# Kernel optimization log

Measured on AMD Instinct MI355X. Metric: run time of the kernel, lower is better.

Reference implementation:

```python
import jax, jax.numpy as jnp
import numpy as np

S = 1024; VOCAB = 100000; EMB = 300
POS_SZ = 64; CHAR_E = 50; CHAR_ENC = 128; WLEN = 16
NCHARS = 100; NPOSTAG = 50; NPOSITIONS = 1024
D = EMB + 3 * POS_SZ + CHAR_ENC  # word_rep_size = 620
BIH = 128   # per-direction LSTM hidden (bilstm_hidden_size // 2)
TLH = 256; LCC = 128; GCC = 256
NET = 8; NTAGS = 16; NREL = 16
TOKF = 2 * BIH + LCC + TLH       # 640
SENTF = 2 * TOKF + GCC           # 1536

def _p(k, shape):
    return 0.02 * jax.random.normal(k, shape, dtype=jnp.float32)

def setup_inputs():
    key = jax.random.key(0)
    ks = jax.random.split(key, 30)
    return {
        'word_inputs': jax.random.randint(ks[0], (1, S), 0, VOCAB),
        'char_inputs': jax.random.randint(ks[1], (1, S, WLEN), 0, NCHARS),
        'postag_inputs': jax.random.randint(ks[2], (1, S), 0, NPOSTAG),
        'dependency_inputs': jax.random.randint(ks[3], (1, S), 0, 64),
        'position_inputs': jax.random.randint(ks[4], (1, S), 0, NPOSITIONS),
        'topo_order': jnp.arange(S),  # children-before-parents order
        'parent': jnp.concatenate([jnp.arange(1, S), jnp.array([S])]),  # chain dep tree; root -> dummy slot S
        'pointed_token_idx': 5,
        'word_table': _p(ks[5], (VOCAB, EMB)),
        'char_table': _p(ks[6], (NCHARS, CHAR_E)),
        'char_conv_w': _p(ks[7], (CHAR_ENC, CHAR_E, 3)),
        'char_conv_b': jnp.zeros((CHAR_ENC,), jnp.float32),
        'postag_table': _p(ks[8], (NPOSTAG, POS_SZ)),
        'position_table': _p(ks[9], (NPOSITIONS, POS_SZ)),
        'lstm_f_Wx': _p(ks[10], (D, 4 * BIH)),
        'lstm_f_Wh': _p(ks[11], (BIH, 4 * BIH)),
        'lstm_f_b': jnp.zeros((4 * BIH,), jnp.float32),
        'lstm_b_Wx': _p(ks[12], (D, 4 * BIH)),
        'lstm_b_Wh': _p(ks[13], (BIH, 4 * BIH)),
        'lstm_b_b': jnp.zeros((4 * BIH,), jnp.float32),
        'word_cnn_w': _p(ks[14], (LCC, D, 3)),
        'word_cnn_b': jnp.zeros((LCC,), jnp.float32),
        'tl_Wiou': _p(ks[15], (D, 3 * TLH)),
        'tl_Uiou': _p(ks[16], (TLH, 3 * TLH)),
        'tl_biou': jnp.zeros((3 * TLH,), jnp.float32),
        'tl_Wf': _p(ks[17], (D, TLH)),
        'tl_Uf': _p(ks[18], (TLH, TLH)),
        'tl_bf': jnp.zeros((TLH,), jnp.float32),
        'sent_cnn_w': _p(ks[19], (GCC, D, 3)),
        'sent_cnn_b': jnp.zeros((GCC,), jnp.float32),
        'et_w': _p(ks[20], (GCC + TOKF, NET)),
        'et_b': jnp.zeros((NET,), jnp.float32),
        'crf_w': _p(ks[21], (SENTF, NTAGS)),
        'crf_b': jnp.zeros((NTAGS,), jnp.float32),
        'crf_trans': _p(ks[22], (NTAGS, NTAGS)),
        'rel_w': _p(ks[23], (SENTF, NREL)),
        'rel_b': jnp.zeros((NREL,), jnp.float32),
    }

def _conv1d(x, w, b):
    # x: [N, Cin, W], w: [Cout, Cin, K], padding=1 (matches nn.Conv1d(..., padding=1))
    y = jax.lax.conv_general_dilated(x, w, (1,), [(1, 1)], dimension_numbers=('NCW', 'OIW', 'NCW'))
    return y + b[None, :, None]

def _lstm(xs, Wx, Wh, b):
    H = Wh.shape[0]
    def step(carry, x):
        h, c = carry
        g = x @ Wx + h @ Wh + b
        i, f, gg, o = jnp.split(g, 4, axis=-1)
        c = jax.nn.sigmoid(f) * c + jax.nn.sigmoid(i) * jnp.tanh(gg)
        h = jax.nn.sigmoid(o) * jnp.tanh(c)
        return (h, c), h
    init = (jnp.zeros((H,), xs.dtype), jnp.zeros((H,), xs.dtype))
    _, hs = jax.lax.scan(step, init, xs)
    return hs

def _tree_lstm(x, order, parent, Wiou, Uiou, biou, Wf, Uf, bf):
    # ChildSum TreeLSTM over the whole dependency tree in topological order.
    # Equivalent to the source's per-token subtree recursion: each node's h
    # only depends on its subtree.
    Sn, H = x.shape[0], Uf.shape[0]
    xiou = x @ Wiou + biou                 # [S, 3H]
    xf = jnp.concatenate([x @ Wf + bf, jnp.zeros((1, H), x.dtype)], axis=0)  # dummy row for root's parent
    def step(carry, j):
        h, hsum, fcsum = carry
        iou = xiou[j] + hsum[j] @ Uiou
        i, o, u = jnp.split(iou, 3)
        cj = jax.nn.sigmoid(i) * jnp.tanh(u) + fcsum[j]
        hj = jax.nn.sigmoid(o) * jnp.tanh(cj)
        p = parent[j]
        f = jax.nn.sigmoid(xf[p] + hj @ Uf)  # per-child forget gate
        return (h.at[j].set(hj), hsum.at[p].add(hj), fcsum.at[p].add(f * cj)), None
    h0 = jnp.zeros((Sn, H), x.dtype)
    acc0 = jnp.zeros((Sn + 1, H), x.dtype)
    (h, _, _), _ = jax.lax.scan(step, (h0, acc0, acc0), order)
    return h

def _viterbi(emissions, trans):
    # emissions: [S, T]; trans[i, j] = score(i -> j)
    def step(score, e):
        s = score[:, None] + trans
        return jnp.max(s, axis=0) + e, jnp.argmax(s, axis=0)
    final, ptrs = jax.lax.scan(step, emissions[0], emissions[1:])
    last = jnp.argmax(final)
    def bt(tag, p):
        prev = p[tag]
        return prev, prev
    _, prevs = jax.lax.scan(bt, last, ptrs, reverse=True)
    return jnp.concatenate([prevs, last[None]])

def reference(word_inputs, char_inputs, postag_inputs, dependency_inputs, position_inputs, topo_order, parent, pointed_token_idx, word_table, char_table, char_conv_w, char_conv_b, postag_table, position_table, lstm_f_Wx, lstm_f_Wh, lstm_f_b, lstm_b_Wx, lstm_b_Wh, lstm_b_b, word_cnn_w, word_cnn_b, tl_Wiou, tl_Uiou, tl_biou, tl_Wf, tl_Uf, tl_bf, sent_cnn_w, sent_cnn_b, et_w, et_b, crf_w, crf_b, crf_trans, rel_w, rel_b):
    we = word_table[word_inputs]                                   # [1,S,EMB]
    cx = jnp.transpose(char_table[char_inputs[0]], (0, 2, 1))      # [S,CHAR_E,WLEN]
    ce = jnp.max(jax.nn.relu(_conv1d(cx, char_conv_w, char_conv_b)), axis=-1)[None]  # CharCNN -> [1,S,CHAR_ENC]
    pe = postag_table[postag_inputs]
    poe = position_table[position_inputs]
    de = position_table[dependency_inputs]                         # faithful to source bug: uses position table
    inputs = jnp.concatenate([we, ce, pe, poe, de], axis=-1)       # [1,S,D]
    x = inputs[0]
    hf = _lstm(x, lstm_f_Wx, lstm_f_Wh, lstm_f_b)
    hb = _lstm(x[::-1], lstm_b_Wx, lstm_b_Wh, lstm_b_b)[::-1]
    bilstm = jnp.concatenate([hf, hb], axis=-1)[None]              # [1,S,2*BIH]
    xc = jnp.transpose(inputs, (0, 2, 1))                          # [1,D,S]
    local_cnn = jnp.transpose(_conv1d(xc, word_cnn_w, word_cnn_b), (0, 2, 1))
    tree_h = _tree_lstm(x, topo_order, parent, tl_Wiou, tl_Uiou, tl_biou, tl_Wf, tl_Uf, tl_bf)[None]
    global_cnn = jnp.transpose(jnp.max(_conv1d(xc, sent_cnn_w, sent_cnn_b), axis=-1, keepdims=True), (0, 2, 1))  # [1,1,GCC]
    tokens_info = jnp.concatenate([bilstm, local_cnn, tree_h], axis=-1)  # [1,S,TOKF]
    ptr = tokens_info[:, pointed_token_idx, :]                     # [1,TOKF]
    ptr_info = jnp.broadcast_to(ptr[:, None, :], (1, S, TOKF))
    glob_info = jnp.broadcast_to(global_cnn, (1, S, GCC))
    sentence_encoding = jnp.concatenate([tokens_info, ptr_info, glob_info], axis=-1)  # dropout = identity (eval)
    one_vec = jnp.concatenate([global_cnn[:, 0, :], ptr], axis=-1)
    entitytype = jax.nn.softmax(one_vec @ et_w + et_b, axis=-1)
    entities = _viterbi(sentence_encoding[0] @ crf_w + crf_b, crf_trans)
    relations = jax.nn.sigmoid(sentence_encoding @ rel_w + rel_b)
    return sentence_encoding, entitytype, entities, relations
```

## Files before the change

kernel.cpp:

```cpp
#include <hip/hip_runtime.h>
#include <math.h>

#define SEQ   1024
#define DX    620
#define BIH   128
#define TLH   256
#define NTAGS 16

#define O_X      0
#define O_XGF    634880
#define O_XGB    (O_XGF + 524288)
#define O_XIOU   (O_XGB + 524288)
#define O_XF     (O_XIOU + 786432)
#define O_LCNN   (O_XF + 262400)
#define O_SCNN   (O_LCNN + 131072)
#define O_PART   (O_SCNN + 262144)
#define O_GCNN   (O_PART + 4096)
#define O_HF     (O_GCNN + 256)
#define O_HB     (O_HF + 131072)
#define O_TREEH  (O_HB + 131072)
#define O_IOUA   (O_TREEH + 262144)
#define O_FCSUM  (O_IOUA + 787200)
#define O_EMIS   (O_FCSUM + 262400)
#define O_CNT    (O_EMIS + 16384)

#define SENT 0xFFFFFFFFu

__device__ __forceinline__ float sig_f(float x){ return 1.0f/(1.0f + __expf(-x)); }
__device__ __forceinline__ float tanh_f(float x){
  float ax = fabsf(x);
  float e  = __expf(-2.0f*ax);
  float t  = (1.0f - e)/(1.0f + e);
  return x < 0.0f ? -t : t;
}
__device__ __forceinline__ int physslot(int s){ return s ^ ((s>>3)&7); }

__global__ __launch_bounds__(128) void k_embed(
    const int* __restrict__ wi, const int* __restrict__ ci,
    const int* __restrict__ postag_in, const int* __restrict__ dep_in, const int* __restrict__ pos_in,
    const float* __restrict__ word_table, const float* __restrict__ char_table,
    const float* __restrict__ ccw, const float* __restrict__ ccb,
    const float* __restrict__ postag_table, const float* __restrict__ position_table,
    float* __restrict__ x)
{
  int s = blockIdx.x;
  int tid = threadIdx.x;
  __shared__ __align__(16) float ce[50][16];
  for (int idx = tid; idx < 800; idx += 128){
    int e = idx >> 4, t = idx & 15;
    ce[e][t] = char_table[ci[s*16 + t]*50 + e];
  }
  __syncthreads();
  float* xr = x + (size_t)s*DX;
  const float* wrow = word_table + (size_t)wi[s]*300;
  for (int d = tid; d < 300; d += 128) xr[d] = wrow[d];
  {
    int oc = tid;
    const float* wp = ccw + oc*150;
    float acc[16];
    float b = ccb[oc];
    #pragma unroll
    for (int t=0;t<16;t++) acc[t] = b;
    for (int ic=0; ic<50; ic++){
      float w0 = wp[ic*3+0], w1 = wp[ic*3+1], w2 = wp[ic*3+2];
      float cv[16];
      float4 c0 = *(const float4*)&ce[ic][0];
      float4 c1 = *(const float4*)&ce[ic][4];
      float4 c2 = *(const float4*)&ce[ic][8];
      float4 c3 = *(const float4*)&ce[ic][12];
      cv[0]=c0.x;cv[1]=c0.y;cv[2]=c0.z;cv[3]=c0.w;
      cv[4]=c1.x;cv[5]=c1.y;cv[6]=c1.z;cv[7]=c1.w;
      cv[8]=c2.x;cv[9]=c2.y;cv[10]=c2.z;cv[11]=c2.w;
      cv[12]=c3.x;cv[13]=c3.y;cv[14]=c3.z;cv[15]=c3.w;
      #pragma unroll
      for (int t=0;t<16;t++){
        float a = cv[t]*w1;
        if (t > 0)  a += cv[t-1]*w0;
        if (t < 15) a += cv[t+1]*w2;
        acc[t] += a;
      }
    }
    float m = acc[0];
    #pragma unroll
    for (int t=1;t<16;t++) m = fmaxf(m, acc[t]);
    xr[300 + oc] = fmaxf(m, 0.0f);
  }
  if (tid < 64){
    int d = tid;
    xr[428 + d] = postag_table[postag_in[s]*64 + d];
    xr[492 + d] = position_table[pos_in[s]*64 + d];
    xr[556 + d] = position_table[dep_in[s]*64 + d];
  }
}

__device__ __forceinline__ void gemm_tile(
    const float* __restrict__ x, const float* __restrict__ Bm,
    const float* __restrict__ bias, float* __restrict__ C,
    int N, int K, int amode, int bx, int by, int tid,
    float (*As)[64], float (*Bs)[64], int agentc)
{
  int bn = bx*64, bm = by*64;
  int lane = tid & 63, kg = tid >> 6;
  int tx = tid & 15, ty = tid >> 4;
  float acc[4][4] = {{0.f}};
  for (int k0 = 0; k0 < K; k0 += 20){
    #pragma unroll
    for (int kk=0; kk<5; kk++){
      int k = kg*5 + kk;
      float av;
      if (amode == 0){
        av = x[(size_t)(bm+lane)*DX + k0 + k];
      } else {
        int kc = k0 + k;
        int d  = kc/3;
        int sh = kc - d*3 - 1;
        int row = bm + lane + sh;
        av = (row >= 0 && row < SEQ) ? x[(size_t)row*DX + d] : 0.0f;
      }
      As[k][lane] = av;
      Bs[k][lane] = (amode==0) ? Bm[(size_t)(k0+k)*N + bn + lane]
                               : Bm[(size_t)(bn+lane)*K + k0 + k];
    }
    __syncthreads();
    #pragma unroll
    for (int k=0;k<20;k++){
      float4 a = *(const float4*)&As[k][ty<<2];
      float4 b = *(const float4*)&Bs[k][tx<<2];
      acc[0][0]+=a.x*b.x; acc[0][1]+=a.x*b.y; acc[0][2]+=a.x*b.z; acc[0][3]+=a.x*b.w;
      acc[1][0]+=a.y*b.x; acc[1][1]+=a.y*b.y; acc[1][2]+=a.y*b.z; acc[1][3]+=a.y*b.w;
      acc[2][0]+=a.z*b.x; acc[2][1]+=a.z*b.y; acc[2][2]+=a.z*b.z; acc[2][3]+=a.z*b.w;
      acc[3][0]+=a.w*b.x; acc[3][1]+=a.w*b.y; acc[3][2]+=a.w*b.z; acc[3][3]+=a.w*b.w;
    }
    __syncthreads();
  }
  float4 bb;
  bb.x = bias[bn+(tx<<2)+0]; bb.y = bias[bn+(tx<<2)+1];
  bb.z = bias[bn+(tx<<2)+2]; bb.w = bias[bn+(tx<<2)+3];
  #pragma unroll
  for (int i=0;i<4;i++){
    int row = bm + (ty<<2) + i;
    float v0 = acc[i][0]+bb.x, v1 = acc[i][1]+bb.y, v2 = acc[i][2]+bb.z, v3 = acc[i][3]+bb.w;
    if (agentc){
      float* p = &C[(size_t)row*N + bn + (tx<<2)];
      __hip_atomic_store(p+0, v0, __ATOMIC_RELAXED, __HIP_MEMORY_SCOPE_AGENT);
      __hip_atomic_store(p+1, v1, __ATOMIC_RELAXED, __HIP_MEMORY_SCOPE_AGENT);
      __hip_atomic_store(p+2, v2, __ATOMIC_RELAXED, __HIP_MEMORY_SCOPE_AGENT);
      __hip_atomic_store(p+3, v3, __ATOMIC_RELAXED, __HIP_MEMORY_SCOPE_AGENT);
    } else {
      float4 o; o.x=v0; o.y=v1; o.z=v2; o.w=v3;
      *(float4*)&C[(size_t)row*N + bn + (tx<<2)] = o;
    }
  }
}

__global__ __launch_bounds__(256) void k_gmax1(const float* __restrict__ scnn, float* __restrict__ part){
  int b = blockIdx.x, c = threadIdx.x;
  float m = -3.0e38f;
  for (int s = b*64; s < b*64 + 64; s++) m = fmaxf(m, scnn[(size_t)s*256 + c]);
  part[b*256 + c] = m;
}
__global__ __launch_bounds__(256) void k_gmax2(const float* __restrict__ part, float* __restrict__ gcnn){
  int c = threadIdx.x;
  float m = -3.0e38f;
  for (int b=0; b<16; b++) m = fmaxf(m, part[b*256 + c]);
  gcnn[c] = m;
}

struct RGemm {
  const float* B[4];
  const float* bias[4];
  float*       C[4];
  int          N[4];
};

__global__ __launch_bounds__(256, 1) void k_recur(
    const float* __restrict__ xg_f, const float* __restrict__ xg_b,
    const float* __restrict__ Wh_f, const float* __restrict__ Wh_b,
    const float* __restrict__ xiou, const float* __restrict__ xf,
    const float* __restrict__ Uiou, const float* __restrict__ Uf,
    const int* __restrict__ order, const int* __restrict__ parent,
    float* __restrict__ hf, float* __restrict__ hb,
    float* tree_h, float* iou_acc, float* fcsum,
    const float* __restrict__ x, RGemm rg_args,
    const float* __restrict__ wcnn_w, const float* __restrict__ wcnn_b,
    const float* __restrict__ scnn_w, const float* __restrict__ scnn_b,
    float* __restrict__ lcnn, float* __restrict__ scnn,
    int* cnt)
{
  int bid = blockIdx.x;
  int tid = threadIdx.x;

  if (bid >= 262){
    __shared__ __align__(16) float As[20][64];
    __shared__ __align__(16) float Bs[20][64];
    int j = bid - 262;
    for (int s=0;s<3;s++){
      int tn = j*3 + s;
      if (tn < 32) gemm_tile(x, wcnn_w, wcnn_b, lcnn, 128, 1860, 1, tn&1, tn>>1, tid, As, Bs, 0);
      else { int t2 = tn-32; gemm_tile(x, scnn_w, scnn_b, scnn, 256, 1860, 1, t2&3, t2>>2, tid, As, Bs, 0); }
      __syncthreads();
    }
    return;
  }

  if (bid >= 6){
    __shared__ __align__(16) float As[20][64];
    __shared__ __align__(16) float Bs[20][64];
    int j = bid - 6;
    for (int s=0;s<2;s++){
      int T = j*2 + s;
      int k = T>>5, r = T&31;
      int z, by, bn;
      if (r < 8)       { z=0; by=k;    bn=r;    }
      else if (r < 16) { z=1; by=15-k; bn=r-8;  }
      else if (r < 28) { z=2; by=k;    bn=r-16; }
      else             { z=3; by=k;    bn=r-28; }
      gemm_tile(x, rg_args.B[z], rg_args.bias[z], rg_args.C[z], rg_args.N[z],
                620, 0, bn, by, tid, As, Bs, 1);
      __syncthreads();
      if (tid == 0)
        __hip_atomic_fetch_add(&cnt[z*16 + by], 1, __ATOMIC_RELEASE, __HIP_MEMORY_SCOPE_AGENT);
      __syncthreads();
    }
    return;
  }

  if (bid >= 4){
    const float* xg  = (bid == 4) ? xg_f : xg_b;
    const float* Wh  = (bid == 4) ? Wh_f : Wh_b;
    float* hout      = (bid == 4) ? hf : hb;
    int zc = (bid == 4) ? 0 : 1;
    int cg = tid >> 1, rg = tid & 1;
    float4 w[4][16];
    #pragma unroll
    for (int cc=0;cc<4;cc++){
      int col = cg*4 + cc;
      #pragma unroll
      for (int r4=0;r4<16;r4++){
        int row = rg*64 + r4*4;
        w[cc][r4].x = Wh[(size_t)(row+0)*512 + col];
        w[cc][r4].y = Wh[(size_t)(row+1)*512 + col];
        w[cc][r4].z = Wh[(size_t)(row+2)*512 + col];
        w[cc][r4].w = Wh[(size_t)(row+3)*512 + col];
      }
    }
    #pragma unroll
    for (int cc=0;cc<4;cc++)
      #pragma unroll
      for (int r4=0;r4<16;r4++)
        asm volatile("" : "+v"(w[cc][r4].x), "+v"(w[cc][r4].y), "+v"(w[cc][r4].z), "+v"(w[cc][r4].w));

    __shared__ __align__(16) float lhl[BIH];
    __shared__ float lcst[BIH];
    __shared__ float gl[512];
    if (tid < BIH){ lhl[tid] = 0.f; lcst[tid] = 0.f; }
    __syncthreads();
    const float4* lhl4 = (const float4*)lhl;

    int Wm = (bid == 4) ? -1 : 16;
    {
      int n0 = (bid == 4) ? 0 : (SEQ-1);
      int g0 = n0 >> 6;
      if (bid == 4){
        for (int g = Wm+1; g <= g0; g++)
          while (__hip_atomic_load(&cnt[zc*16+g], __ATOMIC_ACQUIRE, __HIP_MEMORY_SCOPE_AGENT) < 8)
            __builtin_amdgcn_s_sleep(8);
      } else {
        for (int g = Wm-1; g >= g0; g--)
          while (__hip_atomic_load(&cnt[zc*16+g], __ATOMIC_ACQUIRE, __HIP_MEMORY_SCOPE_AGENT) < 8)
            __builtin_amdgcn_s_sleep(8);
      }
      Wm = g0;
    }
    float4 nxg4 = make_float4(0.f,0.f,0.f,0.f);
    if (rg == 0){
      int n0 = (bid == 4) ? 0 : (SEQ-1);
      nxg4 = *(const float4*)&xg[(size_t)n0*512 + cg*4];
    }
    for (int st=0; st<SEQ; st++){
      int n = (bid == 4) ? st : (SEQ-1-st);
      float4 xg4 = nxg4;
      if (st+1 < SEQ){
        int n1 = (bid == 4) ? (st+1) : (SEQ-2-st);
        int g1 = n1 >> 6;
        if (bid == 4){
          if (g1 > Wm){
            for (int g = Wm+1; g <= g1; g++)
              while (__hip_atomic_load(&cnt[zc*16+g], __ATOMIC_ACQUIRE, __HIP_MEMORY_SCOPE_AGENT) < 8)
                __builtin_amdgcn_s_sleep(8);
            Wm = g1;
          }
        } else {
          if (g1 < Wm){
            for (int g = Wm-1; g >= g1; g--)
              while (__hip_atomic_load(&cnt[zc*16+g], __ATOMIC_ACQUIRE, __HIP_MEMORY_SCOPE_AGENT) < 8)
                __builtin_amdgcn_s_sleep(8);
            Wm = g1;
          }
        }
        if (rg == 0) nxg4 = *(const float4*)&xg[(size_t)n1*512 + cg*4];
      }
      float acc[4] = {0.f,0.f,0.f,0.f};
      #pragma unroll
      for (int r4=0;r4<16;r4++){
        float4 h4 = lhl4[rg*16 + r4];
        #pragma unroll
        for (int cc=0;cc<4;cc++)
          acc[cc] += h4.x*w[cc][r4].x + h4.y*w[cc][r4].y + h4.z*w[cc][r4].z + h4.w*w[cc][r4].w;
      }
      #pragma unroll
      for (int cc=0;cc<4;cc++) acc[cc] += __shfl_xor(acc[cc], 1);
      if (rg == 0){
        float4 o = make_float4(acc[0]+xg4.x, acc[1]+xg4.y, acc[2]+xg4.z, acc[3]+xg4.w);
        *(float4*)&gl[cg*4] = o;
      }
      __syncthreads();
      if (tid < BIH){
        float gi = gl[tid], gf = gl[BIH+tid], gg = gl[2*BIH+tid], go = gl[3*BIH+tid];
        float c = sig_f(gf)*lcst[tid] + sig_f(gi)*tanh_f(gg);
        float h = sig_f(go)*tanh_f(c);
        lcst[tid] = c;
        lhl[tid] = h;
        hout[(size_t)n*BIH + tid] = h;
      }
      __syncthreads();
    }
    return;
  }

  int blk = bid;
  int cg = tid >> 3, rg = tid & 7;
  int ulo = blk*64;
  float4 w[8][8];
  #pragma unroll
  for (int cc=0;cc<8;cc++){
    int c = cg*8 + cc;
    const float* Wsrc; size_t stride; int gcol;
    if (c < 192){ Wsrc = Uiou; stride = 768; gcol = (c>>6)*TLH + ulo + (c&63); }
    else        { Wsrc = Uf;   stride = 256; gcol = ulo + (c-192); }
    #pragma unroll
    for (int r4=0;r4<8;r4++){
      int row = rg*32 + r4*4;
      w[cc][r4].x = Wsrc[(size_t)(row+0)*stride + gcol];
      w[cc][r4].y = Wsrc[(size_t)(row+1)*stride + gcol];
      w[cc][r4].z = Wsrc[(size_t)(row+2)*stride + gcol];
      w[cc][r4].w = Wsrc[(size_t)(row+3)*stride + gcol];
    }
  }
  #pragma unroll
  for (int cc=0;cc<8;cc++)
    #pragma unroll
    for (int r4=0;r4<8;r4++)
      asm volatile("" : "+v"(w[cc][r4].x), "+v"(w[cc][r4].y), "+v"(w[cc][r4].z), "+v"(w[cc][r4].w));

  __shared__ __align__(16) float hl[TLH];
  __shared__ float colsum[TLH];
  __shared__ float cprev[64];
  __shared__ int ord_l[SEQ];
  __shared__ int par_l[SEQ];
  for (int i=tid; i<SEQ; i+=256){ ord_l[i] = order[i]; par_l[i] = parent[i]; }
  __syncthreads();
  const float4* hl4 = (const float4*)hl;

  int Wm = -1;
  float nxi=0.f, nxo=0.f, nxu=0.f, nxf=0.f;
  if (tid < 64){
    int n0 = ord_l[0];
    int need = n0 >> 6;
    for (int g = 0; g <= need; g++){
      while (__hip_atomic_load(&cnt[32+g], __ATOMIC_ACQUIRE, __HIP_MEMORY_SCOPE_AGENT) < 12)
        __builtin_amdgcn_s_sleep(8);
      while (__hip_atomic_load(&cnt[48+g], __ATOMIC_ACQUIRE, __HIP_MEMORY_SCOPE_AGENT) < 4)
        __builtin_amdgcn_s_sleep(8);
    }
    Wm = need;
    int uu = ulo + tid;
    nxi = xiou[(size_t)n0*768 + uu];
    nxo = xiou[(size_t)n0*768 + 256 + uu];
    nxu = xiou[(size_t)n0*768 + 512 + uu];
  }

  for (int t=0; t<SEQ; t++){
    int n  = ord_l[t];
    int m  = (t > 0) ? ord_l[t-1] : 0;
    int pp = (t > 0) ? par_l[m] : -1;
    bool ppeq = (pp == n);

    float xi=nxi, xo=nxo, xu=nxu, xfv=nxf;
    float ac_i=0.f, ac_o=0.f, ac_u=0.f, fcn=0.f;
    float po_i=0.f, po_o=0.f, po_u=0.f, po_f=0.f;
    if (tid < 64){
      int uu = ulo + tid;
      if (t+1 < SEQ){
        int n1 = ord_l[t+1];
        int pr = par_l[n];
        int need = n1 >> 6;
        if (pr < SEQ && (pr>>6) > need) need = pr>>6;
        if (need > Wm){
          for (int g = Wm+1; g <= need; g++){
            while (__hip_atomic_load(&cnt[32+g], __ATOMIC_ACQUIRE, __HIP_MEMORY_SCOPE_AGENT) < 12)
              __builtin_amdgcn_s_sleep(8);
            while (__hip_atomic_load(&cnt[48+g], __ATOMIC_ACQUIRE, __HIP_MEMORY_SCOPE_AGENT) < 4)
              __builtin_amdgcn_s_sleep(8);
          }
          Wm = need;
        }
        nxi = xiou[(size_t)n1*768 + uu];
        nxo = xiou[(size_t)n1*768 + 256 + uu];
        nxu = xiou[(size_t)n1*768 + 512 + uu];
        nxf = xf[(size_t)pr*256 + uu];
      }
      ac_i = iou_acc[(size_t)n*768 + uu];
      ac_o = iou_acc[(size_t)n*768 + 256 + uu];
      ac_u = iou_acc[(size_t)n*768 + 512 + uu];
      fcn  = fcsum[(size_t)n*256 + uu];
      if (t > 0 && !ppeq){
        po_i = iou_acc[(size_t)pp*768 + uu];
        po_o = iou_acc[(size_t)pp*768 + 256 + uu];
        po_u = iou_acc[(size_t)pp*768 + 512 + uu];
        po_f = fcsum[(size_t)pp*256 + uu];
      }
    }

    if (t > 0){
      float acc[8] = {0.f,0.f,0.f,0.f,0.f,0.f,0.f,0.f};
      int base = rg << 3;
      #pragma unroll
      for (int r4=0;r4<8;r4++){
        float4 h4 = hl4[base + (r4 ^ rg)];
        #pragma unroll
        for (int cc=0;cc<8;cc++)
          acc[cc] += h4.x*w[cc][r4].x + h4.y*w[cc][r4].y + h4.z*w[cc][r4].z + h4.w*w[cc][r4].w;
      }
      #pragma unroll
      for (int cc=0;cc<8;cc++){
        acc[cc] += __shfl_xor(acc[cc], 1);
        acc[cc] += __shfl_xor(acc[cc], 2);
        acc[cc] += __shfl_xor(acc[cc], 4);
      }
      if (rg == 0){
        *(float4*)&colsum[cg*8]     = make_float4(acc[0], acc[1], acc[2], acc[3]);
        *(float4*)&colsum[cg*8 + 4] = make_float4(acc[4], acc[5], acc[6], acc[7]);
      }
    }
    __syncthreads();

    if (tid < 64){
      int uu = ulo + tid;
      float ai = ac_i, ao = ac_o, au = ac_u, fcs = fcn;
      if (t > 0){
        float vi = colsum[tid], vo = colsum[64+tid], vuu = colsum[128+tid], vf = colsum[192+tid];
        float fg  = sig_f(xfv + vf);
        float fcc = fg * cprev[tid];
        if (ppeq){
          ai += vi; ao += vo; au += vuu; fcs += fcc;
        } else {
          iou_acc[(size_t)pp*768 + uu]       = po_i + vi;
          iou_acc[(size_t)pp*768 + 256 + uu] = po_o + vo;
          iou_acc[(size_t)pp*768 + 512 + uu] = po_u + vuu;
          fcsum[(size_t)pp*256 + uu]         = po_f + fcc;
        }
      }
      float cc = sig_f(xi + ai)*tanh_f(xu + au) + fcs;
      float hh = sig_f(xo + ao)*tanh_f(cc);
      cprev[tid] = cc;
      int s = uu >> 2;
      hl[physslot(s)*4 + (uu & 3)] = hh;
      __hip_atomic_store(&tree_h[(size_t)n*TLH + uu], hh, __ATOMIC_RELAXED, __HIP_MEMORY_SCOPE_AGENT);
    } else {
      int p  = tid - 64;
      int fi = (p < ulo) ? p : p + 64;
      const unsigned* tp = (const unsigned*)(tree_h + (size_t)n*TLH + fi);
      unsigned v = __hip_atomic_load(tp, __ATOMIC_RELAXED, __HIP_MEMORY_SCOPE_AGENT);
      while (v == SENT){
        __builtin_amdgcn_s_sleep(1);
        v = __hip_atomic_load(tp, __ATOMIC_RELAXED, __HIP_MEMORY_SCOPE_AGENT);
      }
      hl[physslot(fi>>2)*4 + (fi&3)] = __uint_as_float(v);
    }
    __syncthreads();
  }
}

__global__ __launch_bounds__(256) void k_assemble(
    const float* __restrict__ hf, const float* __restrict__ hb,
    const float* __restrict__ lcnn, const float* __restrict__ tree_h,
    const float* __restrict__ gcnn,
    const float* __restrict__ crf_w, const float* __restrict__ crf_b,
    const float* __restrict__ rel_w, const float* __restrict__ rel_b,
    const int* __restrict__ ptk,
    float* __restrict__ se_out, float* __restrict__ emis, float* __restrict__ rel_out)
{
  int s = blockIdx.x, tid = threadIdx.x;
  int p = ptk[0];
  __shared__ float se[1536];
  for (int d = tid; d < 1536; d += 256){
    float v;
    if      (d < 128)  v = hf[(size_t)s*128 + d];
    else if (d < 256)  v = hb[(size_t)s*128 + d-128];
    else if (d < 384)  v = lcnn[(size_t)s*128 + d-256];
    else if (d < 640)  v = tree_h[(size_t)s*256 + d-384];
    else if (d < 768)  v = hf[(size_t)p*128 + d-640];
    else if (d < 896)  v = hb[(size_t)p*128 + d-768];
    else if (d < 1024) v = lcnn[(size_t)p*128 + d-896];
    else if (d < 1280) v = tree_h[(size_t)p*256 + d-1024];
    else               v = gcnn[d-1280];
    se[d] = v;
    se_out[(size_t)s*1536 + d] = v;
  }
  __syncthreads();
  int o = tid >> 3, l = tid & 7;
  const float* W = (o < 16) ? crf_w : rel_w;
  int oc = (o < 16) ? o : (o - 16);
  float a = 0.f;
  for (int k = l; k < 1536; k += 8) a += se[k]*W[(size_t)k*16 + oc];
  for (int off = 4; off; off >>= 1) a += __shfl_down(a, off, 8);
  if (l == 0){
    if (o < 16) emis[(size_t)s*16 + o] = a + crf_b[o];
    else        rel_out[(size_t)s*16 + oc] = sig_f(a + rel_b[oc]);
  }
}

__global__ __launch_bounds__(256) void k_entity(
    const float* __restrict__ hf, const float* __restrict__ hb,
    const float* __restrict__ lcnn, const float* __restrict__ tree_h,
    const float* __restrict__ gcnn,
    const float* __restrict__ et_w, const float* __restrict__ et_b,
    const int* __restrict__ ptk, float* __restrict__ out_et)
{
  __shared__ float ov[896];
  __shared__ float lg[8];
  int tid = threadIdx.x;
  int p = ptk[0];
  for (int d = tid; d < 896; d += 256){
    float v;
    if      (d < 256) v = gcnn[d];
    else if (d < 384) v = hf[(size_t)p*128 + d-256];
    else if (d < 512) v = hb[(size_t)p*128 + d-384];
    else if (d < 640) v = lcnn[(size_t)p*128 + d-512];
    else              v = tree_h[(size_t)p*256 + d-640];
    ov[d] = v;
  }
  __syncthreads();
  int o = tid >> 5, l = tid & 31;
  float a = 0.f;
  for (int k = l; k < 896; k += 32) a += ov[k]*et_w[(size_t)k*8 + o];
  for (int off = 16; off; off >>= 1) a += __shfl_down(a, off, 32);
  if (l == 0) lg[o] = a + et_b[o];
  __syncthreads();
  if (tid == 0){
    float mx = lg[0];
    for (int i=1;i<8;i++) mx = fmaxf(mx, lg[i]);
    float e[8], sum = 0.f;
    for (int i=0;i<8;i++){ e[i] = __expf(lg[i]-mx); sum += e[i]; }
    for (int i=0;i<8;i++) out_et[i] = e[i]/sum;
  }
}

__global__ __launch_bounds__(64) void k_viterbi(
    const float* __restrict__ emis, const float* __restrict__ trans, float* __restrict__ out_e)
{
  __shared__ __align__(16) float ring[64][16];
  __shared__ unsigned char ptrs[1023*16];
  __shared__ float scL[16];
  int l = threadIdx.x;
  int j = l >> 2, iq = l & 3;
  float tr0 = trans[(iq*4+0)*16 + j];
  float tr1 = trans[(iq*4+1)*16 + j];
  float tr2 = trans[(iq*4+2)*16 + j];
  float tr3 = trans[(iq*4+3)*16 + j];
  {
    const float* src = &emis[(size_t)l*16];
    float4 a = *(const float4*)(src+0), b = *(const float4*)(src+4);
    float4 c = *(const float4*)(src+8), d = *(const float4*)(src+12);
    *(float4*)&ring[l][0] = a;  *(float4*)&ring[l][4] = b;
    *(float4*)&ring[l][8] = c;  *(float4*)&ring[l][12] = d;
  }
  float cur = ring[0][j];
  float sc0 = __shfl(cur, (iq*4+0)<<2, 64);
  float sc1 = __shfl(cur, (iq*4+1)<<2, 64);
  float sc2 = __shfl(cur, (iq*4+2)<<2, 64);
  float sc3 = __shfl(cur, (iq*4+3)<<2, 64);
  float myfinal = cur;
  for (int t=1; t<1024; t++){
    if ((t & 63) == 0){
      const float* src = &emis[(size_t)(t+l)*16];
      float4 a = *(const float4*)(src+0), b = *(const float4*)(src+4);
      float4 c = *(const float4*)(src+8), d = *(const float4*)(src+12);
      int rr = (t+l) & 63;
      *(float4*)&ring[rr][0] = a;  *(float4*)&ring[rr][4] = b;
      *(float4*)&ring[rr][8] = c;  *(float4*)&ring[rr][12] = d;
    }
    float v0 = sc0 + tr0, v1 = sc1 + tr1, v2 = sc2 + tr2, v3 = sc3 + tr3;
    float best = v0; int barg = iq*4;
    if (v1 > best){ best = v1; barg = iq*4+1; }
    if (v2 > best){ best = v2; barg = iq*4+2; }
    if (v3 > best){ best = v3; barg = iq*4+3; }
    float ob = __shfl_down(best, 1, 4); int oa = __shfl_down(barg, 1, 4);
    if (ob > best){ best = ob; barg = oa; }
    ob = __shfl_down(best, 2, 4); oa = __shfl_down(barg, 2, 4);
    if (ob > best){ best = ob; barg = oa; }
    float ns = 0.f;
    if (iq == 0){
      ns = best + ring[t & 63][j];
      ptrs[(t-1)*16 + j] = (unsigned char)barg;
      myfinal = ns;
    }
    sc0 = __shfl(ns, (iq*4+0)<<2, 64);
    sc1 = __shfl(ns, (iq*4+1)<<2, 64);
    sc2 = __shfl(ns, (iq*4+2)<<2, 64);
    sc3 = __shfl(ns, (iq*4+3)<<2, 64);
  }
  if (iq == 0) scL[j] = myfinal;
  if (l == 0){
    float b = scL[0]; int last = 0;
    #pragma unroll
    for (int i=1;i<16;i++){ if (scL[i] > b){ b = scL[i]; last = i; } }
    out_e[1023] = (float)last;
    int cur2 = last;
    for (int t=1022; t>=0; t--){ cur2 = (int)ptrs[t*16 + cur2]; out_e[t] = (float)cur2; }
  }
}

extern "C" void kernel_launch(void* const* d_in, const int* in_sizes, int n_in,
                              void* d_out, int out_size, void* d_ws, size_t ws_size,
                              hipStream_t stream)
{
  (void)in_sizes; (void)n_in; (void)out_size; (void)ws_size;
  const int*   wi         = (const int*)d_in[0];
  const int*   ci         = (const int*)d_in[1];
  const int*   postag_in  = (const int*)d_in[2];
  const int*   dep_in     = (const int*)d_in[3];
  const int*   pos_in     = (const int*)d_in[4];
  const int*   order      = (const int*)d_in[5];
  const int*   parent     = (const int*)d_in[6];
  const int*   ptk        = (const int*)d_in[7];
  const float* word_table = (const float*)d_in[8];
  const float* char_table = (const float*)d_in[9];
  const float* ccw        = (const float*)d_in[10];
  const float* ccb        = (const float*)d_in[11];
  const float* postag_tab = (const float*)d_in[12];
  const float* pos_tab    = (const float*)d_in[13];
  const float* Wx_f       = (const float*)d_in[14];
  const float* Wh_f       = (const float*)d_in[15];
  const float* b_f        = (const float*)d_in[16];
  const float* Wx_b       = (const float*)d_in[17];
  const float* Wh_b       = (const float*)d_in[18];
  const float* b_b        = (const float*)d_in[19];
  const float* wcnn_w     = (const float*)d_in[20];
  const float* wcnn_b     = (const float*)d_in[21];
  const float* Wiou       = (const float*)d_in[22];
  const float* Uiou       = (const float*)d_in[23];
  const float* biou       = (const float*)d_in[24];
  const float* Wf_t       = (const float*)d_in[25];
  const float* Uf_t       = (const float*)d_in[26];
  const float* bf_t       = (const float*)d_in[27];
  const float* scnn_w     = (const float*)d_in[28];
  const float* scnn_b     = (const float*)d_in[29];
  const float* et_w       = (const float*)d_in[30];
  const float* et_b       = (const float*)d_in[31];
  const float* crf_w      = (const float*)d_in[32];
  const float* crf_b      = (const float*)d_in[33];
  const float* crf_trans  = (const float*)d_in[34];
  const float* rel_w      = (const float*)d_in[35];
  const float* rel_b      = (const float*)d_in[36];

  float* ws = (float*)d_ws;
  float* x      = ws + O_X;
  float* xg_f   = ws + O_XGF;
  float* xg_b   = ws + O_XGB;
  float* xiou   = ws + O_XIOU;
  float* xf     = ws + O_XF;
  float* lcnn   = ws + O_LCNN;
  float* scnn   = ws + O_SCNN;
  float* part   = ws + O_PART;
  float* gcnn   = ws + O_GCNN;
  float* hf     = ws + O_HF;
  float* hb     = ws + O_HB;
  float* tree_h = ws + O_TREEH;
  float* iou_acc= ws + O_IOUA;
  float* fcsum  = ws + O_FCSUM;
  float* emis   = ws + O_EMIS;
  int*   cnt    = (int*)(ws + O_CNT);

  float* outF     = (float*)d_out;
  float* se_out   = outF;
  float* et_out   = outF + 1572864;
  float* ent_out  = outF + 1572872;
  float* rel_out  = outF + 1573896;

  hipMemsetAsync(xf, 0, (size_t)1025*256*sizeof(float), stream);
  hipMemsetAsync(iou_acc, 0, ((size_t)1025*768 + 1025*256)*sizeof(float), stream);
  hipMemsetAsync(tree_h, 0xFF, (size_t)1024*256*sizeof(float), stream);
  hipMemsetAsync(cnt, 0, 256, stream);

  k_embed<<<SEQ, 128, 0, stream>>>(wi, ci, postag_in, dep_in, pos_in,
                                   word_table, char_table, ccw, ccb,
                                   postag_tab, pos_tab, x);

  RGemm rga;
  rga.B[0]=Wx_f;  rga.bias[0]=b_f;   rga.C[0]=xg_f; rga.N[0]=512;
  rga.B[1]=Wx_b;  rga.bias[1]=b_b;   rga.C[1]=xg_b; rga.N[1]=512;
  rga.B[2]=Wiou;  rga.bias[2]=biou;  rga.C[2]=xiou; rga.N[2]=768;
  rga.B[3]=Wf_t;  rga.bias[3]=bf_t;  rga.C[3]=xf;   rga.N[3]=256;

  k_recur<<<294, 256, 0, stream>>>(xg_f, xg_b, Wh_f, Wh_b, xiou, xf, Uiou, Uf_t,
                                   order, parent, hf, hb, tree_h, iou_acc, fcsum,
                                   x, rga, wcnn_w, wcnn_b, scnn_w, scnn_b, lcnn, scnn,
                                   cnt);

  k_gmax1<<<16, 256, 0, stream>>>(scnn, part);
  k_gmax2<<<1, 256, 0, stream>>>(part, gcnn);

  k_assemble<<<SEQ, 256, 0, stream>>>(hf, hb, lcnn, tree_h, gcnn,
                                      crf_w, crf_b, rel_w, rel_b, ptk,
                                      se_out, emis, rel_out);

  k_entity<<<1, 256, 0, stream>>>(hf, hb, lcnn, tree_h, gcnn, et_w, et_b, ptk, et_out);

  k_viterbi<<<1, 64, 0, stream>>>(emis, crf_trans, ent_out);
}
```

Measured before the change: 2.717 ms.

## Fuse embedding and global max into persistent recurrent kernel with counter-based dataflow

Moves the embedding computation into the persistent k_recur kernel as extra blocks that publish per-64-token completion counters. The input-projection and CNN GEMM tiles now wait on those counters instead of a kernel boundary, so the recurrences can start as soon as their first token groups are ready. The global max-pool becomes a single block inside the same kernel that waits on a CNN tile counter. The entity softmax is folded into k_assemble as an extra block. Together these remove several launches and let work overlap across stages, at the cost of more spin-waits and a grid of 807 blocks that relies on forward progress of the producer blocks.

```diff
diff --git a/kernel.cpp b/kernel.cpp
--- a/kernel.cpp
+++ b/kernel.cpp
@@ -24,6 +24,13 @@
 #define O_EMIS   (O_FCSUM + 262400)
 #define O_CNT    (O_EMIS + 16384)
 
+#define C_XGF  0
+#define C_XGB  16
+#define C_XIOU 32
+#define C_XF   48
+#define C_X    64
+#define C_SCNN 80
+
 #define SENT 0xFFFFFFFFu
 
 __device__ __forceinline__ float sig_f(float x){ return 1.0f/(1.0f + __expf(-x)); }
@@ -35,62 +42,9 @@
 }
 __device__ __forceinline__ int physslot(int s){ return s ^ ((s>>3)&7); }
 
-__global__ __launch_bounds__(128) void k_embed(
-    const int* __restrict__ wi, const int* __restrict__ ci,
-    const int* __restrict__ postag_in, const int* __restrict__ dep_in, const int* __restrict__ pos_in,
-    const float* __restrict__ word_table, const float* __restrict__ char_table,
-    const float* __restrict__ ccw, const float* __restrict__ ccb,
-    const float* __restrict__ postag_table, const float* __restrict__ position_table,
-    float* __restrict__ x)
-{
-  int s = blockIdx.x;
-  int tid = threadIdx.x;
-  __shared__ __align__(16) float ce[50][16];
-  for (int idx = tid; idx < 800; idx += 128){
-    int e = idx >> 4, t = idx & 15;
-    ce[e][t] = char_table[ci[s*16 + t]*50 + e];
-  }
-  __syncthreads();
-  float* xr = x + (size_t)s*DX;
-  const float* wrow = word_table + (size_t)wi[s]*300;
-  for (int d = tid; d < 300; d += 128) xr[d] = wrow[d];
-  {
-    int oc = tid;
-    const float* wp = ccw + oc*150;
-    float acc[16];
-    float b = ccb[oc];
-    #pragma unroll
-    for (int t=0;t<16;t++) acc[t] = b;
-    for (int ic=0; ic<50; ic++){
-      float w0 = wp[ic*3+0], w1 = wp[ic*3+1], w2 = wp[ic*3+2];
-      float cv[16];
-      float4 c0 = *(const float4*)&ce[ic][0];
-      float4 c1 = *(const float4*)&ce[ic][4];
-      float4 c2 = *(const float4*)&ce[ic][8];
-      float4 c3 = *(const float4*)&ce[ic][12];
-      cv[0]=c0.x;cv[1]=c0.y;cv[2]=c0.z;cv[3]=c0.w;
-      cv[4]=c1.x;cv[5]=c1.y;cv[6]=c1.z;cv[7]=c1.w;
-      cv[8]=c2.x;cv[9]=c2.y;cv[10]=c2.z;cv[11]=c2.w;
-      cv[12]=c3.x;cv[13]=c3.y;cv[14]=c3.z;cv[15]=c3.w;
-      #pragma unroll
-      for (int t=0;t<16;t++){
-        float a = cv[t]*w1;
-        if (t > 0)  a += cv[t-1]*w0;
-        if (t < 15) a += cv[t+1]*w2;
-        acc[t] += a;
-      }
-    }
-    float m = acc[0];
-    #pragma unroll
-    for (int t=1;t<16;t++) m = fmaxf(m, acc[t]);
-    xr[300 + oc] = fmaxf(m, 0.0f);
-  }
-  if (tid < 64){
-    int d = tid;
-    xr[428 + d] = postag_table[postag_in[s]*64 + d];
-    xr[492 + d] = position_table[pos_in[s]*64 + d];
-    xr[556 + d] = position_table[dep_in[s]*64 + d];
-  }
+__device__ __forceinline__ void wait_cnt(int* cnt, int idx, int target){
+  while (__hip_atomic_load(&cnt[idx], __ATOMIC_ACQUIRE, __HIP_MEMORY_SCOPE_AGENT) < target)
+    __builtin_amdgcn_s_sleep(8);
 }
 
 __device__ __forceinline__ void gemm_tile(
@@ -153,19 +107,6 @@
   }
 }
 
-__global__ __launch_bounds__(256) void k_gmax1(const float* __restrict__ scnn, float* __restrict__ part){
-  int b = blockIdx.x, c = threadIdx.x;
-  float m = -3.0e38f;
-  for (int s = b*64; s < b*64 + 64; s++) m = fmaxf(m, scnn[(size_t)s*256 + c]);
-  part[b*256 + c] = m;
-}
-__global__ __launch_bounds__(256) void k_gmax2(const float* __restrict__ part, float* __restrict__ gcnn){
-  int c = threadIdx.x;
-  float m = -3.0e38f;
-  for (int b=0; b<16; b++) m = fmaxf(m, part[b*256 + c]);
-  gcnn[c] = m;
-}
-
 struct RGemm {
   const float* B[4];
   const float* bias[4];
@@ -174,6 +115,11 @@
 };
 
 __global__ __launch_bounds__(256, 1) void k_recur(
+    const int* __restrict__ wi, const int* __restrict__ ci,
+    const int* __restrict__ postag_in, const int* __restrict__ dep_in, const int* __restrict__ pos_in,
+    const float* __restrict__ word_table, const float* __restrict__ char_table,
+    const float* __restrict__ ccw, const float* __restrict__ ccb,
+    const float* __restrict__ postag_tab, const float* __restrict__ pos_tab,
     const float* __restrict__ xg_f, const float* __restrict__ xg_b,
     const float* __restrict__ Wh_f, const float* __restrict__ Wh_b,
     const float* __restrict__ xiou, const float* __restrict__ xf,
@@ -181,32 +127,45 @@
     const int* __restrict__ order, const int* __restrict__ parent,
     float* __restrict__ hf, float* __restrict__ hb,
     float* tree_h, float* iou_acc, float* fcsum,
-    const float* __restrict__ x, RGemm rg_args,
+    float* __restrict__ x, RGemm rg_args,
     const float* __restrict__ wcnn_w, const float* __restrict__ wcnn_b,
     const float* __restrict__ scnn_w, const float* __restrict__ scnn_b,
-    float* __restrict__ lcnn, float* __restrict__ scnn,
+    float* __restrict__ lcnn, float* __restrict__ scnn, float* __restrict__ gcnn,
     int* cnt)
 {
   int bid = blockIdx.x;
   int tid = threadIdx.x;
 
-  if (bid >= 262){
+  if (bid >= 775){
     __shared__ __align__(16) float As[20][64];
     __shared__ __align__(16) float Bs[20][64];
-    int j = bid - 262;
+    int j = bid - 775;
     for (int s=0;s<3;s++){
       int tn = j*3 + s;
-      if (tn < 32) gemm_tile(x, wcnn_w, wcnn_b, lcnn, 128, 1860, 1, tn&1, tn>>1, tid, As, Bs, 0);
-      else { int t2 = tn-32; gemm_tile(x, scnn_w, scnn_b, scnn, 256, 1860, 1, t2&3, t2>>2, tid, As, Bs, 0); }
+      int by = (tn < 32) ? (tn>>1) : ((tn-32)>>2);
+      if (tid == 0){
+        int glo = by > 0 ? by-1 : 0, ghi = by < 15 ? by+1 : 15;
+        for (int g = glo; g <= ghi; g++) wait_cnt(cnt, C_X + g, 32);
+      }
       __syncthreads();
+      if (tn < 32){
+        gemm_tile(x, wcnn_w, wcnn_b, lcnn, 128, 1860, 1, tn&1, by, tid, As, Bs, 0);
+      } else {
+        int t2 = tn - 32;
+        gemm_tile(x, scnn_w, scnn_b, scnn, 256, 1860, 1, t2&3, by, tid, As, Bs, 0);
+        __syncthreads();
+        if (tid == 0)
+          __hip_atomic_fetch_add(&cnt[C_SCNN], 1, __ATOMIC_RELEASE, __HIP_MEMORY_SCOPE_AGENT);
+      }
+      __syncthreads();
     }
     return;
   }
 
-  if (bid >= 6){
+  if (bid >= 519){
     __shared__ __align__(16) float As[20][64];
     __shared__ __align__(16) float Bs[20][64];
-    int j = bid - 6;
+    int j = bid - 519;
     for (int s=0;s<2;s++){
       int T = j*2 + s;
       int k = T>>5, r = T&31;
@@ -215,6 +174,8 @@
       else if (r < 16) { z=1; by=15-k; bn=r-8;  }
       else if (r < 28) { z=2; by=k;    bn=r-16; }
       else             { z=3; by=k;    bn=r-28; }
+      if (tid == 0) wait_cnt(cnt, C_X + by, 32);
+      __syncthreads();
       gemm_tile(x, rg_args.B[z], rg_args.bias[z], rg_args.C[z], rg_args.N[z],
                 620, 0, bn, by, tid, As, Bs, 1);
       __syncthreads();
@@ -222,6 +183,74 @@
         __hip_atomic_fetch_add(&cnt[z*16 + by], 1, __ATOMIC_RELEASE, __HIP_MEMORY_SCOPE_AGENT);
       __syncthreads();
     }
+    return;
+  }
+
+  if (bid >= 7){
+    int j   = bid - 7;
+    int tok = j*2 + (tid >> 7);
+    int lt  = tid & 127;
+    __shared__ __align__(16) float ce2[2][50][16];
+    float (*ce)[16] = ce2[tid >> 7];
+    for (int idx = lt; idx < 800; idx += 128){
+      int e = idx >> 4, t = idx & 15;
+      ce[e][t] = char_table[ci[tok*16 + t]*50 + e];
+    }
+    __syncthreads();
+    float* xr = x + (size_t)tok*DX;
+    const float* wrow = word_table + (size_t)wi[tok]*300;
+    for (int d = lt; d < 300; d += 128) xr[d] = wrow[d];
+    {
+      int oc = lt;
+      const float* wp = ccw + oc*150;
+      float acc[16];
+      float b = ccb[oc];
+      #pragma unroll
+      for (int t=0;t<16;t++) acc[t] = b;
+      for (int ic=0; ic<50; ic++){
+        float w0 = wp[ic*3+0], w1 = wp[ic*3+1], w2 = wp[ic*3+2];
+        float cv[16];
+        float4 c0 = *(const float4*)&ce[ic][0];
+        float4 c1 = *(const float4*)&ce[ic][4];
+        float4 c2 = *(const float4*)&ce[ic][8];
+        float4 c3 = *(const float4*)&ce[ic][12];
+        cv[0]=c0.x;cv[1]=c0.y;cv[2]=c0.z;cv[3]=c0.w;
+        cv[4]=c1.x;cv[5]=c1.y;cv[6]=c1.z;cv[7]=c1.w;
+        cv[8]=c2.x;cv[9]=c2.y;cv[10]=c2.z;cv[11]=c2.w;
+        cv[12]=c3.x;cv[13]=c3.y;cv[14]=c3.z;cv[15]=c3.w;
+        #pragma unroll
+        for (int t=0;t<16;t++){
+          float a = cv[t]*w1;
+          if (t > 0)  a += cv[t-1]*w0;
+          if (t < 15) a += cv[t+1]*w2;
+          acc[t] += a;
+        }
+      }
+      float m = acc[0];
+      #pragma unroll
+      for (int t=1;t<16;t++) m = fmaxf(m, acc[t]);
+      xr[300 + oc] = fmaxf(m, 0.0f);
+    }
+    if (lt < 64){
+      int d = lt;
+      xr[428 + d] = postag_tab[postag_in[tok]*64 + d];
+      xr[492 + d] = pos_tab[pos_in[tok]*64 + d];
+      xr[556 + d] = pos_tab[dep_in[tok]*64 + d];
+    }
+    __syncthreads();
+    if (tid == 0)
+      __hip_atomic_fetch_add(&cnt[C_X + ((j*2) >> 6)], 1, __ATOMIC_RELEASE, __HIP_MEMORY_SCOPE_AGENT);
+    return;
+  }
+
+  if (bid == 6){
+    if (tid == 0) wait_cnt(cnt, C_SCNN, 64);
+    __syncthreads();
+    int c = tid;
+    float m = -3.0e38f;
+    #pragma unroll 8
+    for (int s = 0; s < SEQ; s++) m = fmaxf(m, scnn[(size_t)s*256 + c]);
+    gcnn[c] = m;
     return;
   }
 
@@ -261,15 +290,11 @@
     {
       int n0 = (bid == 4) ? 0 : (SEQ-1);
       int g0 = n0 >> 6;
-      if (bid == 4){
-        for (int g = Wm+1; g <= g0; g++)
-          while (__hip_atomic_load(&cnt[zc*16+g], __ATOMIC_ACQUIRE, __HIP_MEMORY_SCOPE_AGENT) < 8)
-            __builtin_amdgcn_s_sleep(8);
-      } else {
-        for (int g = Wm-1; g >= g0; g--)
-          while (__hip_atomic_load(&cnt[zc*16+g], __ATOMIC_ACQUIRE, __HIP_MEMORY_SCOPE_AGENT) < 8)
-            __builtin_amdgcn_s_sleep(8);
-      }
+      if (tid == 0){
+        if (bid == 4){ for (int g = 0; g <= g0; g++) wait_cnt(cnt, zc*16+g, 8); }
+        else         { for (int g = 15; g >= g0; g--) wait_cnt(cnt, zc*16+g, 8); }
+      }
+      __syncthreads();
       Wm = g0;
     }
     float4 nxg4 = make_float4(0.f,0.f,0.f,0.f);
@@ -283,20 +308,10 @@
       if (st+1 < SEQ){
         int n1 = (bid == 4) ? (st+1) : (SEQ-2-st);
         int g1 = n1 >> 6;
-        if (bid == 4){
-          if (g1 > Wm){
-            for (int g = Wm+1; g <= g1; g++)
-              while (__hip_atomic_load(&cnt[zc*16+g], __ATOMIC_ACQUIRE, __HIP_MEMORY_SCOPE_AGENT) < 8)
-                __builtin_amdgcn_s_sleep(8);
-            Wm = g1;
-          }
-        } else {
-          if (g1 < Wm){
-            for (int g = Wm-1; g >= g1; g--)
-              while (__hip_atomic_load(&cnt[zc*16+g], __ATOMIC_ACQUIRE, __HIP_MEMORY_SCOPE_AGENT) < 8)
-                __builtin_amdgcn_s_sleep(8);
-            Wm = g1;
-          }
+        if (g1 != Wm){
+          if (tid == 0) wait_cnt(cnt, zc*16+g1, 8);
+          __syncthreads();
+          Wm = g1;
         }
         if (rg == 0) nxg4 = *(const float4*)&xg[(size_t)n1*512 + cg*4];
       }
@@ -364,20 +379,23 @@
 
   int Wm = -1;
   float nxi=0.f, nxo=0.f, nxu=0.f, nxf=0.f;
-  if (tid < 64){
+  {
     int n0 = ord_l[0];
     int need = n0 >> 6;
-    for (int g = 0; g <= need; g++){
-      while (__hip_atomic_load(&cnt[32+g], __ATOMIC_ACQUIRE, __HIP_MEMORY_SCOPE_AGENT) < 12)
-        __builtin_amdgcn_s_sleep(8);
-      while (__hip_atomic_load(&cnt[48+g], __ATOMIC_ACQUIRE, __HIP_MEMORY_SCOPE_AGENT) < 4)
-        __builtin_amdgcn_s_sleep(8);
-    }
+    if (tid == 0){
+      for (int g = 0; g <= need; g++){
+        wait_cnt(cnt, C_XIOU + g, 12);
+        wait_cnt(cnt, C_XF + g, 4);
+      }
+    }
+    __syncthreads();
     Wm = need;
-    int uu = ulo + tid;
-    nxi = xiou[(size_t)n0*768 + uu];
-    nxo = xiou[(size_t)n0*768 + 256 + uu];
-    nxu = xiou[(size_t)n0*768 + 512 + uu];
+    if (tid < 64){
+      int uu = ulo + tid;
+      nxi = xiou[(size_t)n0*768 + uu];
+      nxo = xiou[(size_t)n0*768 + 256 + uu];
+      nxu = xiou[(size_t)n0*768 + 512 + uu];
+    }
   }
 
   for (int t=0; t<SEQ; t++){
@@ -385,6 +403,24 @@
     int m  = (t > 0) ? ord_l[t-1] : 0;
     int pp = (t > 0) ? par_l[m] : -1;
     bool ppeq = (pp == n);
+
+    int need = -1;
+    if (t+1 < SEQ){
+      int n1 = ord_l[t+1];
+      int pr = par_l[n];
+      need = n1 >> 6;
+      if (pr < SEQ && (pr>>6) > need) need = pr>>6;
+      if (need > Wm){
+        if (tid == 0){
+          for (int g = Wm+1; g <= need; g++){
+            wait_cnt(cnt, C_XIOU + g, 12);
+            wait_cnt(cnt, C_XF + g, 4);
+          }
+        }
+        __syncthreads();
+        Wm = need;
+      }
+    }
 
     float xi=nxi, xo=nxo, xu=nxu, xfv=nxf;
     float ac_i=0.f, ac_o=0.f, ac_u=0.f, fcn=0.f;
@@ -394,17 +430,6 @@
       if (t+1 < SEQ){
         int n1 = ord_l[t+1];
         int pr = par_l[n];
-        int need = n1 >> 6;
-        if (pr < SEQ && (pr>>6) > need) need = pr>>6;
-        if (need > Wm){
-          for (int g = Wm+1; g <= need; g++){
-            while (__hip_atomic_load(&cnt[32+g], __ATOMIC_ACQUIRE, __HIP_MEMORY_SCOPE_AGENT) < 12)
-              __builtin_amdgcn_s_sleep(8);
-            while (__hip_atomic_load(&cnt[48+g], __ATOMIC_ACQUIRE, __HIP_MEMORY_SCOPE_AGENT) < 4)
-              __builtin_amdgcn_s_sleep(8);
-          }
-          Wm = need;
-        }
         nxi = xiou[(size_t)n1*768 + uu];
         nxo = xiou[(size_t)n1*768 + 256 + uu];
         nxu = xiou[(size_t)n1*768 + 512 + uu];
@@ -467,7 +492,7 @@
       int s = uu >> 2;
       hl[physslot(s)*4 + (uu & 3)] = hh;
       __hip_atomic_store(&tree_h[(size_t)n*TLH + uu], hh, __ATOMIC_RELAXED, __HIP_MEMORY_SCOPE_AGENT);
-    } else {
+    } else if (tid >= 64 && tid < 256){
       int p  = tid - 64;
       int fi = (p < ulo) ? p : p + 64;
       const unsigned* tp = (const unsigned*)(tree_h + (size_t)n*TLH + fi);
@@ -488,11 +513,42 @@
     const float* __restrict__ gcnn,
     const float* __restrict__ crf_w, const float* __restrict__ crf_b,
     const float* __restrict__ rel_w, const float* __restrict__ rel_b,
+    const float* __restrict__ et_w, const float* __restrict__ et_b,
     const int* __restrict__ ptk,
-    float* __restrict__ se_out, float* __restrict__ emis, float* __restrict__ rel_out)
+    float* __restrict__ se_out, float* __restrict__ emis, float* __restrict__ rel_out,
+    float* __restrict__ out_et)
 {
-  int s = blockIdx.x, tid = threadIdx.x;
+  int tid = threadIdx.x;
   int p = ptk[0];
+  if (blockIdx.x == SEQ){
+    __shared__ float ov[896];
+    __shared__ float lg[8];
+    for (int d = tid; d < 896; d += 256){
+      float v;
+      if      (d < 256) v = gcnn[d];
+      else if (d < 384) v = hf[(size_t)p*128 + d-256];
+      else if (d < 512) v = hb[(size_t)p*128 + d-384];
+      else if (d < 640) v = lcnn[(size_t)p*128 + d-512];
+      else              v = tree_h[(size_t)p*256 + d-640];
+      ov[d] = v;
+    }
+    __syncthreads();
+    int o = tid >> 5, l = tid & 31;
+    float a = 0.f;
+    for (int k = l; k < 896; k += 32) a += ov[k]*et_w[(size_t)k*8 + o];
+    for (int off = 16; off; off >>= 1) a += __shfl_down(a, off, 32);
+    if (l == 0) lg[o] = a + et_b[o];
+    __syncthreads();
+    if (tid == 0){
+      float mx = lg[0];
+      for (int i=1;i<8;i++) mx = fmaxf(mx, lg[i]);
+      float e[8], sum = 0.f;
+      for (int i=0;i<8;i++){ e[i] = __expf(lg[i]-mx); sum += e[i]; }
+      for (int i=0;i<8;i++) out_et[i] = e[i]/sum;
+    }
+    return;
+  }
+  int s = blockIdx.x;
   __shared__ float se[1536];
   for (int d = tid; d < 1536; d += 256){
     float v;
@@ -518,42 +574,6 @@
   if (l == 0){
     if (o < 16) emis[(size_t)s*16 + o] = a + crf_b[o];
     else        rel_out[(size_t)s*16 + oc] = sig_f(a + rel_b[oc]);
-  }
-}
-
-__global__ __launch_bounds__(256) void k_entity(
-    const float* __restrict__ hf, const float* __restrict__ hb,
-    const float* __restrict__ lcnn, const float* __restrict__ tree_h,
-    const float* __restrict__ gcnn,
-    const float* __restrict__ et_w, const float* __restrict__ et_b,
-    const int* __restrict__ ptk, float* __restrict__ out_et)
-{
-  __shared__ float ov[896];
-  __shared__ float lg[8];
-  int tid = threadIdx.x;
-  int p = ptk[0];
-  for (int d = tid; d < 896; d += 256){
-    float v;
-    if      (d < 256) v = gcnn[d];
-    else if (d < 384) v = hf[(size_t)p*128 + d-256];
-    else if (d < 512) v = hb[(size_t)p*128 + d-384];
-    else if (d < 640) v = lcnn[(size_t)p*128 + d-512];
-    else              v = tree_h[(size_t)p*256 + d-640];
-    ov[d] = v;
-  }
-  __syncthreads();
-  int o = tid >> 5, l = tid & 31;
-  float a = 0.f;
-  for (int k = l; k < 896; k += 32) a += ov[k]*et_w[(size_t)k*8 + o];
-  for (int off = 16; off; off >>= 1) a += __shfl_down(a, off, 32);
-  if (l == 0) lg[o] = a + et_b[o];
-  __syncthreads();
-  if (tid == 0){
-    float mx = lg[0];
-    for (int i=1;i<8;i++) mx = fmaxf(mx, lg[i]);
-    float e[8], sum = 0.f;
-    for (int i=0;i<8;i++){ e[i] = __expf(lg[i]-mx); sum += e[i]; }
-    for (int i=0;i<8;i++) out_et[i] = e[i]/sum;
   }
 }
 
@@ -673,7 +693,6 @@
   float* xf     = ws + O_XF;
   float* lcnn   = ws + O_LCNN;
   float* scnn   = ws + O_SCNN;
-  float* part   = ws + O_PART;
   float* gcnn   = ws + O_GCNN;
   float* hf     = ws + O_HF;
   float* hb     = ws + O_HB;
@@ -692,11 +711,7 @@
   hipMemsetAsync(xf, 0, (size_t)1025*256*sizeof(float), stream);
   hipMemsetAsync(iou_acc, 0, ((size_t)1025*768 + 1025*256)*sizeof(float), stream);
   hipMemsetAsync(tree_h, 0xFF, (size_t)1024*256*sizeof(float), stream);
-  hipMemsetAsync(cnt, 0, 256, stream);
-
-  k_embed<<<SEQ, 128, 0, stream>>>(wi, ci, postag_in, dep_in, pos_in,
-                                   word_table, char_table, ccw, ccb,
-                                   postag_tab, pos_tab, x);
+  hipMemsetAsync(cnt, 0, 512, stream);
 
   RGemm rga;
   rga.B[0]=Wx_f;  rga.bias[0]=b_f;   rga.C[0]=xg_f; rga.N[0]=512;
@@ -704,19 +719,17 @@
   rga.B[2]=Wiou;  rga.bias[2]=biou;  rga.C[2]=xiou; rga.N[2]=768;
   rga.B[3]=Wf_t;  rga.bias[3]=bf_t;  rga.C[3]=xf;   rga.N[3]=256;
 
-  k_recur<<<294, 256, 0, stream>>>(xg_f, xg_b, Wh_f, Wh_b, xiou, xf, Uiou, Uf_t,
+  k_recur<<<807, 256, 0, stream>>>(wi, ci, postag_in, dep_in, pos_in,
+                                   word_table, char_table, ccw, ccb,
+                                   postag_tab, pos_tab,
+                                   xg_f, xg_b, Wh_f, Wh_b, xiou, xf, Uiou, Uf_t,
                                    order, parent, hf, hb, tree_h, iou_acc, fcsum,
-                                   x, rga, wcnn_w, wcnn_b, scnn_w, scnn_b, lcnn, scnn,
-                                   cnt);
-
-  k_gmax1<<<16, 256, 0, stream>>>(scnn, part);
-  k_gmax2<<<1, 256, 0, stream>>>(part, gcnn);
-
-  k_assemble<<<SEQ, 256, 0, stream>>>(hf, hb, lcnn, tree_h, gcnn,
-                                      crf_w, crf_b, rel_w, rel_b, ptk,
-                                      se_out, emis, rel_out);
-
-  k_entity<<<1, 256, 0, stream>>>(hf, hb, lcnn, tree_h, gcnn, et_w, et_b, ptk, et_out);
+                                   x, rga, wcnn_w, wcnn_b, scnn_w, scnn_b,
+                                   lcnn, scnn, gcnn, cnt);
+
+  k_assemble<<<SEQ+1, 256, 0, stream>>>(hf, hb, lcnn, tree_h, gcnn,
+                                        crf_w, crf_b, rel_w, rel_b, et_w, et_b, ptk,
+                                        se_out, emis, rel_out, et_out);
 
   k_viterbi<<<1, 64, 0, stream>>>(emis, crf_trans, ent_out);
 }
```

Measured after the change: 2.787 ms. +2.6%, slower.
